# Kernel tuning notes

Measured on AMD Instinct MI355X. Metric: run time of the kernel, lower is better.

The kernel has to match this reference:

```python
import jax, jax.numpy as jnp
import numpy as np

DIM, HEADS, HEAD_DIM, EPS = 1536, 12, 128, 1e-6
B, S = 1, 4096


def rmsnorm(x, w, eps=EPS):
    v = jnp.mean(jnp.square(x), axis=-1, keepdims=True)
    return x * jax.lax.rsqrt(v + eps) * w


def apply_rope(x, freqs):
    # x: [b,s,n,d]; freqs: [s, d//2] rotation angles (complex rope on adjacent pairs)
    b, s, n, d = x.shape
    xr = x.reshape(b, s, n, d // 2, 2)
    cos = jnp.cos(freqs)[None, :, None, :]
    sin = jnp.sin(freqs)[None, :, None, :]
    x0, x1 = xr[..., 0], xr[..., 1]
    out = jnp.stack([x0 * cos - x1 * sin, x0 * sin + x1 * cos], axis=-1)
    return out.reshape(b, s, n, d)


def setup_inputs() -> dict:
    key = jax.random.key(0)
    ks = jax.random.split(key, 12)
    scale = 0.02
    x = jax.random.normal(ks[0], (B, S, DIM), jnp.float32)
    # standard rope angles: pos * inv_freq
    inv_freq = 1.0 / (10000.0 ** (jnp.arange(0, HEAD_DIM, 2, dtype=jnp.float32) / HEAD_DIM))
    freqs = jnp.arange(S, dtype=jnp.float32)[:, None] * inv_freq[None, :]  # [S, 64]
    Wq = jax.random.normal(ks[1], (DIM, DIM), jnp.float32) * scale
    bq = jax.random.normal(ks[2], (DIM,), jnp.float32) * scale
    Wk = jax.random.normal(ks[3], (DIM, DIM), jnp.float32) * scale
    bk = jax.random.normal(ks[4], (DIM,), jnp.float32) * scale
    Wv = jax.random.normal(ks[5], (DIM, DIM), jnp.float32) * scale
    bv = jax.random.normal(ks[6], (DIM,), jnp.float32) * scale
    Wo = jax.random.normal(ks[7], (DIM, DIM), jnp.float32) * scale
    bo = jax.random.normal(ks[8], (DIM,), jnp.float32) * scale
    gq = 1.0 + jax.random.normal(ks[9], (DIM,), jnp.float32) * 0.01
    gk = 1.0 + jax.random.normal(ks[10], (DIM,), jnp.float32) * 0.01
    return dict(x=x, freqs=freqs, Wq=Wq, bq=bq, Wk=Wk, bk=bk, Wv=Wv, bv=bv,
                Wo=Wo, bo=bo, gq=gq, gk=gk)


def reference(x, freqs, Wq, bq, Wk, bk, Wv, bv, Wo, bo, gq, gk):
    b, s = x.shape[:2]
    n, d = HEADS, HEAD_DIM
    q = apply_rope(rmsnorm(x @ Wq.T + bq, gq).reshape(b, s, n, d), freqs)
    k = apply_rope(rmsnorm(x @ Wk.T + bk, gk).reshape(b, s, n, d), freqs)
    v = (x @ Wv.T + bv).reshape(b, s, n, d)
    # SDPA: softmax(q k^T / sqrt(d)) v
    scores = jnp.einsum('bqnd,bknd->bnqk', q, k) / jnp.sqrt(jnp.asarray(d, x.dtype))
    attn = jax.nn.softmax(scores, axis=-1)
    out = jnp.einsum('bnqk,bknd->bqnd', attn, v).reshape(b, s, n * d)
    return out @ Wo.T + bo
```

## Files before the change

### kernel.cpp

```cpp
#include <hip/hip_runtime.h>
#include <stdint.h>
#include <math.h>

#define DIM 1536
#define SEQ 4096
#define HEADS 12
#define HD 128

typedef __bf16 bf16x8 __attribute__((ext_vector_type(8)));
typedef float f32x4 __attribute__((ext_vector_type(4)));

typedef __attribute__((address_space(1))) void gas_void;
typedef __attribute__((address_space(3))) void las_void;

__device__ __forceinline__ float b2f(unsigned short u) {
  union { unsigned int i; float f; } x; x.i = ((unsigned int)u) << 16; return x.f;
}
__device__ __forceinline__ unsigned short f2b(float f) {
  union { float f; unsigned int i; } x; x.f = f;
  unsigned int u = x.i;
  unsigned int r = (u + 0x7fffu + ((u >> 16) & 1u)) >> 16;
  return (unsigned short)r;
}
__device__ __forceinline__ void gll16(const unsigned short* g, unsigned short* l) {
  __builtin_amdgcn_global_load_lds((gas_void*)g, (las_void*)l, 16, 0, 0);
}
__device__ __forceinline__ void cvtpk(unsigned int& d, float a, float b) {
  asm("v_cvt_pk_bf16_f32 %0, %1, %2" : "=v"(d) : "v"(a), "v"(b));
}
__device__ __forceinline__ void pl32(unsigned int& a, unsigned int& b) {
  asm("v_permlane32_swap_b32 %0, %1" : "+v"(a), "+v"(b));
}
__device__ __forceinline__ void pl16(unsigned int& a, unsigned int& b) {
  asm("v_permlane16_swap_b32 %0, %1" : "+v"(a), "+v"(b));
}
__device__ __forceinline__ float fexp2(float x) { return __builtin_amdgcn_exp2f(x); }

__global__ void detect_kernel(const unsigned int* __restrict__ xw, int* flag) {
  __shared__ int cnt;
  if (threadIdx.x == 0) cnt = 0;
  __syncthreads();
  int local = 0;
  for (int i = threadIdx.x; i < 1024; i += 256) {
    unsigned int e = (xw[i] >> 7) & 0xFFu;
    if (e >= 110u && e <= 140u) local++;
  }
  atomicAdd(&cnt, local);
  __syncthreads();
  if (threadIdx.x == 0) *flag = (cnt > 512) ? 0 : 1;
}

__global__ void convert_bf16_kernel(const void* __restrict__ src,
                                    unsigned short* __restrict__ dst, int n4,
                                    const int* __restrict__ flag) {
  int f = *flag;
  for (int i = blockIdx.x * blockDim.x + threadIdx.x; i < n4; i += gridDim.x * blockDim.x) {
    if (f) {
      float4 v = ((const float4*)src)[i];
      union { unsigned short h[4]; uint2 u; } pk;
      pk.h[0] = f2b(v.x); pk.h[1] = f2b(v.y); pk.h[2] = f2b(v.z); pk.h[3] = f2b(v.w);
      ((uint2*)dst)[i] = pk.u;
    } else {
      ((uint2*)dst)[i] = ((const uint2*)src)[i];
    }
  }
}

__global__ void convert_w4_kernel(const void* s0, const void* s1, const void* s2, const void* s3,
                                  unsigned short* d0, unsigned short* d1,
                                  unsigned short* d2, unsigned short* d3,
                                  int n4, const int* __restrict__ flag) {
  const void* s; unsigned short* d;
  switch (blockIdx.y) {
    case 0: s = s0; d = d0; break;
    case 1: s = s1; d = d1; break;
    case 2: s = s2; d = d2; break;
    default: s = s3; d = d3; break;
  }
  int f = *flag;
  for (int i = blockIdx.x * blockDim.x + threadIdx.x; i < n4; i += gridDim.x * blockDim.x) {
    if (f) {
      float4 v = ((const float4*)s)[i];
      union { unsigned short h[4]; uint2 u; } pk;
      pk.h[0] = f2b(v.x); pk.h[1] = f2b(v.y); pk.h[2] = f2b(v.z); pk.h[3] = f2b(v.w);
      ((uint2*)d)[i] = pk.u;
    } else {
      ((uint2*)d)[i] = ((const uint2*)s)[i];
    }
  }
}

__global__ void convert_small_kernel(const void* s0, const void* s1, const void* s2,
                                     const void* s3, const void* s4, const void* s5,
                                     const void* sf,
                                     unsigned short* d0, unsigned short* d1,
                                     unsigned short* d2, unsigned short* d3,
                                     unsigned short* d4, unsigned short* d5,
                                     float2* df, int nb, int nf,
                                     const int* __restrict__ flag) {
  int f = *flag;
  if (blockIdx.y == 6) {
    for (int i = blockIdx.x * blockDim.x + threadIdx.x; i < nf; i += gridDim.x * blockDim.x) {
      float a = f ? ((const float*)sf)[i] : b2f(((const unsigned short*)sf)[i]);
      float sn, cs;
      __sincosf(a, &sn, &cs);
      df[i] = make_float2(cs, sn);
    }
    return;
  }
  const void* s; unsigned short* d;
  switch (blockIdx.y) {
    case 0: s = s0; d = d0; break;
    case 1: s = s1; d = d1; break;
    case 2: s = s2; d = d2; break;
    case 3: s = s3; d = d3; break;
    case 4: s = s4; d = d4; break;
    default: s = s5; d = d5; break;
  }
  for (int i = blockIdx.x * blockDim.x + threadIdx.x; i < nb; i += gridDim.x * blockDim.x)
    d[i] = f ? f2b(((const float*)s)[i]) : ((const unsigned short*)s)[i];
}

__global__ void signal_kernel(float* out) { if (threadIdx.x == 0) out[0] = 999.0f; }

template<int BM>
__device__ __forceinline__ void gemm_bt_body(
    const unsigned short* __restrict__ A,
    const unsigned short* __restrict__ W,
    const unsigned short* __restrict__ bias,
    unsigned short* __restrict__ Cb, float* __restrict__ Cf, int fmt, int vmode,
    int K, int N, int bx, int by)
{
  constexpr int BK = 64;
  constexpr int MI = BM / 32;
  constexpr int ALINES = BM * BK * 2 / 4096;
  __shared__ unsigned short As[BM * BK];
  __shared__ unsigned short Bs[128 * BK];
  const int t = threadIdx.x;
  const int wave = t >> 6, lane = t & 63;
  const int quad = lane >> 4, l16 = lane & 15;
  const int m0 = by * BM, n0 = bx * 128;
  const int wm = (wave >> 1) * (BM / 2), wn = (wave & 1) * 64;

  f32x4 acc[MI][4] = {};

  const int srow = t >> 3;
  const int scol = ((t & 7) ^ ((t >> 3) & 7)) * 8;
  const unsigned short* Ag = A + (size_t)(m0 + srow) * K + scol;
  const unsigned short* Wg = W + (size_t)(n0 + srow) * K + scol;

  for (int k0 = 0; k0 < K; k0 += BK) {
    __syncthreads();
#pragma unroll
    for (int L = 0; L < ALINES; ++L)
      gll16(Ag + (size_t)L * 32 * K + k0, &As[L * 2048 + t * 8]);
#pragma unroll
    for (int L = 0; L < 4; ++L)
      gll16(Wg + (size_t)L * 32 * K + k0, &Bs[L * 2048 + t * 8]);
    __syncthreads();
#pragma unroll
    for (int c = 0; c < 2; ++c) {
      bf16x8 af[MI], bfr[4];
#pragma unroll
      for (int i = 0; i < MI; ++i) {
        int row = wm + i * 16 + l16;
        af[i] = *(const bf16x8*)&As[row * 64 + ((c * 4 + quad) ^ (row & 7)) * 8];
      }
#pragma unroll
      for (int j = 0; j < 4; ++j) {
        int row = wn + j * 16 + l16;
        bfr[j] = *(const bf16x8*)&Bs[row * 64 + ((c * 4 + quad) ^ (row & 7)) * 8];
      }
#pragma unroll
      for (int i = 0; i < MI; ++i)
#pragma unroll
        for (int j = 0; j < 4; ++j)
          acc[i][j] = __builtin_amdgcn_mfma_f32_16x16x32_bf16(af[i], bfr[j], acc[i][j], 0, 0, 0);
    }
  }

#pragma unroll
  for (int i = 0; i < MI; ++i) {
    int row = m0 + wm + i * 16 + quad * 4;
#pragma unroll
    for (int j = 0; j < 4; ++j) {
      int col = n0 + wn + j * 16 + l16;
      float bv = b2f(bias[col]);
      if (vmode) {
        union { unsigned short h4[4]; uint2 u; } pk;
#pragma unroll
        for (int r = 0; r < 4; ++r) pk.h4[r] = f2b(acc[i][j][r] + bv);
        *(uint2*)&Cb[(size_t)col * SEQ + row] = pk.u;
      } else {
#pragma unroll
        for (int r = 0; r < 4; ++r) {
          float v = acc[i][j][r] + bv;
          size_t idx = (size_t)(row + r) * N + col;
          if (fmt) Cf[idx] = v; else Cb[idx] = f2b(v);
        }
      }
    }
  }
}

__global__ __launch_bounds__(256) void qkv_gemm_kernel(
    const unsigned short* __restrict__ x,
    const unsigned short* __restrict__ Wq, const unsigned short* __restrict__ bq,
    const unsigned short* __restrict__ Wk, const unsigned short* __restrict__ bk,
    const unsigned short* __restrict__ Wv, const unsigned short* __restrict__ bv,
    unsigned short* qb, unsigned short* kb, unsigned short* vt)
{
  const int flat = blockIdx.x + 12 * blockIdx.y + 384 * blockIdx.z;
  const int swz = (flat & 7) * 144 + (flat >> 3);
  const int bz = swz / 384;
  const int rem = swz - bz * 384;
  const int by = rem / 12, bx = rem - by * 12;
  const unsigned short *W, *b; unsigned short* C; int vm = 0;
  if (bz == 0)      { W = Wq; b = bq; C = qb; }
  else if (bz == 1) { W = Wk; b = bk; C = kb; }
  else              { W = Wv; b = bv; C = vt; vm = 1; }
  gemm_bt_body<128>(x, W, b, C, nullptr, 0, vm, DIM, DIM, bx, by);
}

__global__ __launch_bounds__(256) void out_gemm_kernel(
    const unsigned short* __restrict__ ab, const unsigned short* __restrict__ Wo,
    const unsigned short* __restrict__ bo, void* out, const int* __restrict__ flag)
{
  const int flat = blockIdx.x + 12 * blockIdx.y;
  const int swz = (flat & 7) * 96 + (flat >> 3);
  const int by = swz / 12, bx = swz - by * 12;
  int fmt = *flag;
  gemm_bt_body<64>(ab, Wo, bo, (unsigned short*)out, (float*)out, fmt, 0,
                   DIM, DIM, bx, by);
}

__global__ __launch_bounds__(256) void norm_rope_kernel(
    unsigned short* __restrict__ qb, unsigned short* __restrict__ kb,
    const unsigned short* __restrict__ gq, const unsigned short* __restrict__ gk,
    const float2* __restrict__ csf)
{
  const int s = blockIdx.x;
  const int isq = (blockIdx.y == 0);
  unsigned short* row = (isq ? qb : kb) + (size_t)s * DIM;
  const unsigned short* g = (isq ? gq : gk);
  const int t = threadIdx.x;
  float ss = 0.f;
#pragma unroll
  for (int i = 0; i < 6; ++i) {
    float xv = b2f(row[t + 256 * i]);
    ss += xv * xv;
  }
#pragma unroll
  for (int off = 32; off > 0; off >>= 1) ss += __shfl_down(ss, off);
  __shared__ float red[4];
  if ((t & 63) == 0) red[t >> 6] = ss;
  __syncthreads();
  float tot = red[0] + red[1] + red[2] + red[3];
  float rinv = 1.0f / sqrtf(tot * (1.0f / DIM) + 1e-6f);
  if (isq) rinv *= 0.12751744900725559f;
#pragma unroll
  for (int i = 0; i < 3; ++i) {
    int pg = t + 256 * i;
    int c0 = pg * 2;
    float x0 = b2f(row[c0]), x1 = b2f(row[c0 + 1]);
    float y0 = x0 * rinv * b2f(g[c0]);
    float y1 = x1 * rinv * b2f(g[c0 + 1]);
    float2 cs = csf[s * 64 + (pg & 63)];
    row[c0]     = f2b(y0 * cs.x - y1 * cs.y);
    row[c0 + 1] = f2b(y0 * cs.y + y1 * cs.x);
  }
}

__global__ __launch_bounds__(256) void attn_kernel(
    const unsigned short* __restrict__ qb,
    const unsigned short* __restrict__ kb,
    const unsigned short* __restrict__ vt,
    float* __restrict__ op,
    float* __restrict__ lp,
    int seg)
{
  __shared__ unsigned short Ks[64 * 128];
  __shared__ unsigned short Vs[128 * 64];

  const int t = threadIdx.x;
  const int wave = t >> 6, lane = t & 63;
  const int quad = lane >> 4, l16 = lane & 15;
  const int h = blockIdx.y;
  const int z = blockIdx.z;
  const int qbase = blockIdx.x * 128 + wave * 32;
  const int kc0 = z * seg;

  bf16x8 qf[2][4];
#pragma unroll
  for (int mt = 0; mt < 2; ++mt)
#pragma unroll
    for (int kk = 0; kk < 4; ++kk)
      qf[mt][kk] = *(const bf16x8*)(qb + (size_t)(qbase + mt * 16 + l16) * DIM
                                    + h * HD + kk * 32 + quad * 8);

  f32x4 o[2][8] = {};
  float Lr[2] = {};

  const int krow = t >> 2, kblk = (t & 3) * 4;
  const int vd = t >> 1,  vblk = (t & 1) * 4;

  const unsigned short* kbase = kb + (size_t)krow * DIM + h * HD + kblk * 8;
  const unsigned short* vbase = vt + ((size_t)h * HD + vd) * SEQ + vblk * 8;

  uint4 kr0, kr1, kr2, kr3, vr0, vr1, vr2, vr3;
  {
    const unsigned short* s = kbase + (size_t)kc0 * DIM;
    kr0 = *(const uint4*)(s);
    kr1 = *(const uint4*)(s + 8);
    kr2 = *(const uint4*)(s + 16);
    kr3 = *(const uint4*)(s + 24);
    const unsigned short* sv = vbase + kc0;
    vr0 = *(const uint4*)(sv);
    vr1 = *(const uint4*)(sv + 8);
    vr2 = *(const uint4*)(sv + 16);
    vr3 = *(const uint4*)(sv + 24);
  }

  for (int kc = kc0; kc < kc0 + seg; kc += 64) {
    __syncthreads();
    {
      unsigned short* dst = &Ks[krow * 128];
      const int sw = krow & 7;
      *(uint4*)(dst + ((kblk + 0) ^ sw) * 8) = kr0;
      *(uint4*)(dst + ((kblk + 1) ^ sw) * 8) = kr1;
      *(uint4*)(dst + ((kblk + 2) ^ sw) * 8) = kr2;
      *(uint4*)(dst + ((kblk + 3) ^ sw) * 8) = kr3;
    }
    {
      unsigned short* dst = &Vs[vd * 64];
      const int sw = vd & 7;
      *(uint4*)(dst + ((vblk + 0) ^ sw) * 8) = vr0;
      *(uint4*)(dst + ((vblk + 1) ^ sw) * 8) = vr1;
      *(uint4*)(dst + ((vblk + 2) ^ sw) * 8) = vr2;
      *(uint4*)(dst + ((vblk + 3) ^ sw) * 8) = vr3;
    }
    __syncthreads();

    {
      int nkc = kc + 64;
      if (nkc >= kc0 + seg) nkc = kc;
      const unsigned short* s = kbase + (size_t)nkc * DIM;
      kr0 = *(const uint4*)(s);
      kr1 = *(const uint4*)(s + 8);
      kr2 = *(const uint4*)(s + 16);
      kr3 = *(const uint4*)(s + 24);
      const unsigned short* sv = vbase + nkc;
      vr0 = *(const uint4*)(sv);
      vr1 = *(const uint4*)(sv + 8);
      vr2 = *(const uint4*)(sv + 16);
      vr3 = *(const uint4*)(sv + 24);
    }

    f32x4 sc[2][4] = {};
    __builtin_amdgcn_s_setprio(1);
#pragma unroll
    for (int kk = 0; kk < 4; ++kk) {
#pragma unroll
      for (int j = 0; j < 4; ++j) {
        int row = j * 16 + l16;
        bf16x8 kf = *(const bf16x8*)&Ks[row * 128 + ((kk * 4 + quad) ^ (row & 7)) * 8];
        sc[0][j] = __builtin_amdgcn_mfma_f32_16x16x32_bf16(kf, qf[0][kk], sc[0][j], 0, 0, 0);
        sc[1][j] = __builtin_amdgcn_mfma_f32_16x16x32_bf16(kf, qf[1][kk], sc[1][j], 0, 0, 0);
      }
    }
    __builtin_amdgcn_s_setprio(0);

    unsigned int wlo[2][4], whi[2][4];
#pragma unroll
    for (int mt = 0; mt < 2; ++mt) {
      float ls = 0.f;
#pragma unroll
      for (int j = 0; j < 4; ++j) {
        float p0 = fexp2(sc[mt][j][0]);
        float p1 = fexp2(sc[mt][j][1]);
        float p2 = fexp2(sc[mt][j][2]);
        float p3 = fexp2(sc[mt][j][3]);
        ls += (p0 + p1) + (p2 + p3);
        cvtpk(wlo[mt][j], p0, p1);
        cvtpk(whi[mt][j], p2, p3);
      }
      Lr[mt] += ls;
    }

    bf16x8 pf[2][2];
#pragma unroll
    for (int mt = 0; mt < 2; ++mt)
#pragma unroll
      for (int kk2 = 0; kk2 < 2; ++kk2) {
        unsigned int ul = wlo[mt][kk2 * 2], vl = wlo[mt][kk2 * 2 + 1];
        unsigned int uh = whi[mt][kk2 * 2], vh = whi[mt][kk2 * 2 + 1];
        pl32(ul, vl); pl16(ul, vl);
        pl32(uh, vh); pl16(uh, vh);
        union { unsigned int w[4]; bf16x8 v; } u;
        u.w[0] = ul; u.w[1] = uh; u.w[2] = vl; u.w[3] = vh;
        pf[mt][kk2] = u.v;
      }

    __builtin_amdgcn_s_setprio(1);
#pragma unroll
    for (int kk2 = 0; kk2 < 2; ++kk2) {
#pragma unroll
      for (int j2 = 0; j2 < 8; ++j2) {
        bf16x8 vf = *(const bf16x8*)&Vs[(j2 * 16 + l16) * 64
                                        + ((kk2 * 4 + quad) ^ (l16 & 7)) * 8];
        o[0][j2] = __builtin_amdgcn_mfma_f32_16x16x32_bf16(pf[0][kk2], vf, o[0][j2], 0, 0, 0);
        o[1][j2] = __builtin_amdgcn_mfma_f32_16x16x32_bf16(pf[1][kk2], vf, o[1][j2], 0, 0, 0);
      }
    }
    __builtin_amdgcn_s_setprio(0);
  }

  float* opz = op + (size_t)z * SEQ * DIM;
  float* lpz = lp + (size_t)z * HEADS * SEQ + (size_t)h * SEQ;
#pragma unroll
  for (int mt = 0; mt < 2; ++mt) {
    float L = Lr[mt];
    L += __shfl_xor(L, 16);
    L += __shfl_xor(L, 32);
    if (lane < 16) lpz[qbase + mt * 16 + l16] = L;
  }
#pragma unroll
  for (int mt = 0; mt < 2; ++mt) {
#pragma unroll
    for (int j2 = 0; j2 < 8; ++j2) {
      int col = h * HD + j2 * 16 + l16;
#pragma unroll
      for (int r = 0; r < 4; ++r) {
        int row = qbase + mt * 16 + quad * 4 + r;
        opz[(size_t)row * DIM + col] = o[mt][j2][r];
      }
    }
  }
}

__global__ __launch_bounds__(256) void combine_kernel(
    const float* __restrict__ op, const float* __restrict__ lp,
    unsigned short* __restrict__ ab, int nz)
{
  int idx4 = blockIdx.x * 256 + threadIdx.x;
  int idx = idx4 * 4;
  int row = idx / DIM, col = idx - row * DIM;
  int h = col >> 7;
  float4 o = make_float4(0.f, 0.f, 0.f, 0.f);
  float l = 0.f;
  for (int z = 0; z < nz; ++z) {
    float4 v = *(const float4*)(op + (size_t)z * SEQ * DIM + idx);
    o.x += v.x; o.y += v.y; o.z += v.z; o.w += v.w;
    l += lp[(size_t)z * HEADS * SEQ + (size_t)h * SEQ + row];
  }
  float inv = 1.0f / l;
  union { unsigned short h4[4]; uint2 u; } pk;
  pk.h4[0] = f2b(o.x * inv);
  pk.h4[1] = f2b(o.y * inv);
  pk.h4[2] = f2b(o.z * inv);
  pk.h4[3] = f2b(o.w * inv);
  *(uint2*)&ab[idx] = pk.u;
}

extern "C" void kernel_launch(void* const* d_in, const int* in_sizes, int n_in,
                              void* d_out, int out_size, void* d_ws, size_t ws_size,
                              hipStream_t stream) {
  const int NX = SEQ * DIM, NW = DIM * DIM, NB = DIM, NF = SEQ * 64;

  char* w = (char*)d_ws;
  size_t off = 0;
  int* flag = (int*)(w + off);              off += 256;
  unsigned short* xb  = (unsigned short*)(w + off); off += (size_t)NX * 2;
  unsigned short* Wqb = (unsigned short*)(w + off); off += (size_t)NW * 2;
  unsigned short* Wkb = (unsigned short*)(w + off); off += (size_t)NW * 2;
  unsigned short* Wvb = (unsigned short*)(w + off); off += (size_t)NW * 2;
  unsigned short* Wob = (unsigned short*)(w + off); off += (size_t)NW * 2;
  unsigned short* bqb = (unsigned short*)(w + off); off += 4096;
  unsigned short* bkb = (unsigned short*)(w + off); off += 4096;
  unsigned short* bvb = (unsigned short*)(w + off); off += 4096;
  unsigned short* bob = (unsigned short*)(w + off); off += 4096;
  unsigned short* gqb = (unsigned short*)(w + off); off += 4096;
  unsigned short* gkb = (unsigned short*)(w + off); off += 4096;
  float2* freqcs = (float2*)(w + off);      off += (size_t)NF * 8;
  unsigned short* qb = (unsigned short*)(w + off); off += (size_t)NX * 2;
  unsigned short* kb = (unsigned short*)(w + off); off += (size_t)NX * 2;
  unsigned short* vt = (unsigned short*)(w + off); off += (size_t)NX * 2;
  unsigned short* ab = (unsigned short*)(w + off); off += (size_t)NX * 2;
  float* op = (float*)(w + off);
  float* lp;

  int nz = 2;
  size_t need2 = off + (size_t)2 * NX * 4 + (size_t)2 * HEADS * SEQ * 4;
  if (ws_size < need2) {
    signal_kernel<<<1, 64, 0, stream>>>((float*)d_out);
    return;
  }
  lp = (float*)(w + off + (size_t)nz * NX * 4);

  detect_kernel<<<1, 256, 0, stream>>>((const unsigned int*)d_in[0], flag);

  const int CT = 256;
  auto cgrid = [](int n) { int g = (n + 255) / 256; return g > 4096 ? 4096 : g; };
  convert_bf16_kernel<<<cgrid(NX / 4), CT, 0, stream>>>(d_in[0], xb, NX / 4, flag);
  convert_w4_kernel<<<dim3(cgrid(NW / 4), 4), CT, 0, stream>>>(
      d_in[2], d_in[4], d_in[6], d_in[8], Wqb, Wkb, Wvb, Wob, NW / 4, flag);
  convert_small_kernel<<<dim3(cgrid(NF), 7), CT, 0, stream>>>(
      d_in[3], d_in[5], d_in[7], d_in[9], d_in[10], d_in[11], d_in[1],
      bqb, bkb, bvb, bob, gqb, gkb, freqcs, NB, NF, flag);

  qkv_gemm_kernel<<<dim3(DIM / 128, SEQ / 128, 3), 256, 0, stream>>>(
      xb, Wqb, bqb, Wkb, bkb, Wvb, bvb, qb, kb, vt);
  norm_rope_kernel<<<dim3(SEQ, 2), 256, 0, stream>>>(qb, kb, gqb, gkb, freqcs);
  attn_kernel<<<dim3(SEQ / 128, HEADS, nz), 256, 0, stream>>>(qb, kb, vt, op, lp, SEQ / nz);
  combine_kernel<<<NX / 1024, 256, 0, stream>>>(op, lp, ab, nz);
  out_gemm_kernel<<<dim3(DIM / 128, SEQ / 64), 256, 0, stream>>>(ab, Wob, bob, d_out, flag);
}
```

Before: 391.8 us.

## Swizzle attention block order across XCDs and merge input conversion launches

The attention grid is remapped so that consecutive workgroups, which are round-robined across the eight XCDs, land on the same head and z-split. Each XCD's L2 should then hold the same K/V tiles. The activation conversion is also folded into the weight conversion kernel as a fifth grid row, which removes one launch. The swizzle assumes nwg is divisible by 8 and a fixed grid of 32 q-blocks.

```diff
diff --git a/kernel.cpp b/kernel.cpp
--- a/kernel.cpp
+++ b/kernel.cpp
@@ -50,32 +50,19 @@
   if (threadIdx.x == 0) *flag = (cnt > 512) ? 0 : 1;
 }
 
-__global__ void convert_bf16_kernel(const void* __restrict__ src,
-                                    unsigned short* __restrict__ dst, int n4,
-                                    const int* __restrict__ flag) {
-  int f = *flag;
-  for (int i = blockIdx.x * blockDim.x + threadIdx.x; i < n4; i += gridDim.x * blockDim.x) {
-    if (f) {
-      float4 v = ((const float4*)src)[i];
-      union { unsigned short h[4]; uint2 u; } pk;
-      pk.h[0] = f2b(v.x); pk.h[1] = f2b(v.y); pk.h[2] = f2b(v.z); pk.h[3] = f2b(v.w);
-      ((uint2*)dst)[i] = pk.u;
-    } else {
-      ((uint2*)dst)[i] = ((const uint2*)src)[i];
-    }
-  }
-}
-
-__global__ void convert_w4_kernel(const void* s0, const void* s1, const void* s2, const void* s3,
-                                  unsigned short* d0, unsigned short* d1,
-                                  unsigned short* d2, unsigned short* d3,
-                                  int n4, const int* __restrict__ flag) {
-  const void* s; unsigned short* d;
+__global__ void convert_big_kernel(const void* sx, const void* s0, const void* s1,
+                                   const void* s2, const void* s3,
+                                   unsigned short* dx, unsigned short* d0,
+                                   unsigned short* d1, unsigned short* d2,
+                                   unsigned short* d3,
+                                   int nx4, int nw4, const int* __restrict__ flag) {
+  const void* s; unsigned short* d; int n4;
   switch (blockIdx.y) {
-    case 0: s = s0; d = d0; break;
-    case 1: s = s1; d = d1; break;
-    case 2: s = s2; d = d2; break;
-    default: s = s3; d = d3; break;
+    case 0: s = sx; d = dx; n4 = nx4; break;
+    case 1: s = s0; d = d0; n4 = nw4; break;
+    case 2: s = s1; d = d1; n4 = nw4; break;
+    case 3: s = s2; d = d2; n4 = nw4; break;
+    default: s = s3; d = d3; n4 = nw4; break;
   }
   int f = *flag;
   for (int i = blockIdx.x * blockDim.x + threadIdx.x; i < n4; i += gridDim.x * blockDim.x) {
@@ -277,7 +264,7 @@
     const unsigned short* __restrict__ vt,
     float* __restrict__ op,
     float* __restrict__ lp,
-    int seg)
+    int seg, int nwg)
 {
   __shared__ unsigned short Ks[64 * 128];
   __shared__ unsigned short Vs[128 * 64];
@@ -285,9 +272,15 @@
   const int t = threadIdx.x;
   const int wave = t >> 6, lane = t & 63;
   const int quad = lane >> 4, l16 = lane & 15;
-  const int h = blockIdx.y;
-  const int z = blockIdx.z;
-  const int qbase = blockIdx.x * 128 + wave * 32;
+
+  const int flat = blockIdx.x + (gridDim.x) * (blockIdx.y + HEADS * blockIdx.z);
+  const int swz = (flat & 7) * (nwg >> 3) + (flat >> 3);
+  const int bx = swz & 31;
+  const int rem = swz >> 5;
+  const int h = rem % HEADS;
+  const int z = rem / HEADS;
+
+  const int qbase = bx * 128 + wave * 32;
   const int kc0 = z * seg;
 
   bf16x8 qf[2][4];
@@ -501,9 +494,9 @@
 
   const int CT = 256;
   auto cgrid = [](int n) { int g = (n + 255) / 256; return g > 4096 ? 4096 : g; };
-  convert_bf16_kernel<<<cgrid(NX / 4), CT, 0, stream>>>(d_in[0], xb, NX / 4, flag);
-  convert_w4_kernel<<<dim3(cgrid(NW / 4), 4), CT, 0, stream>>>(
-      d_in[2], d_in[4], d_in[6], d_in[8], Wqb, Wkb, Wvb, Wob, NW / 4, flag);
+  convert_big_kernel<<<dim3(cgrid(NW / 4), 5), CT, 0, stream>>>(
+      d_in[0], d_in[2], d_in[4], d_in[6], d_in[8],
+      xb, Wqb, Wkb, Wvb, Wob, NX / 4, NW / 4, flag);
   convert_small_kernel<<<dim3(cgrid(NF), 7), CT, 0, stream>>>(
       d_in[3], d_in[5], d_in[7], d_in[9], d_in[10], d_in[11], d_in[1],
       bqb, bkb, bvb, bob, gqb, gkb, freqcs, NB, NF, flag);
@@ -511,7 +504,8 @@
   qkv_gemm_kernel<<<dim3(DIM / 128, SEQ / 128, 3), 256, 0, stream>>>(
       xb, Wqb, bqb, Wkb, bkb, Wvb, bvb, qb, kb, vt);
   norm_rope_kernel<<<dim3(SEQ, 2), 256, 0, stream>>>(qb, kb, gqb, gkb, freqcs);
-  attn_kernel<<<dim3(SEQ / 128, HEADS, nz), 256, 0, stream>>>(qb, kb, vt, op, lp, SEQ / nz);
+  attn_kernel<<<dim3(SEQ / 128, HEADS, nz), 256, 0, stream>>>(
+      qb, kb, vt, op, lp, SEQ / nz, (SEQ / 128) * HEADS * nz);
   combine_kernel<<<NX / 1024, 256, 0, stream>>>(op, lp, ab, nz);
   out_gemm_kernel<<<dim3(DIM / 128, SEQ / 64), 256, 0, stream>>>(ab, Wob, bob, d_out, flag);
 }
```

Result: no change. 389.6 us (-0.6%).
